# Optimization experiments

Measured on AMD Instinct MI355X. Metric: run time of the kernel, lower is better.

## Reference

```python
import jax, jax.numpy as jnp
import numpy as np
import math

B, NX, NY = 8, 1024, 1024
DIM_X = DIM_Y = DIM = 1024
H = 8


def layer_norm(x, g, b, eps=1e-5):
    mu = jnp.mean(x, axis=-1, keepdims=True)
    var = jnp.mean(jnp.square(x - mu), axis=-1, keepdims=True)
    return (x - mu) * jax.lax.rsqrt(var + eps) * g + b


def setup_inputs() -> dict:
    key = jax.random.key(0)
    ks = jax.random.split(key, 12)
    s = 1.0 / math.sqrt(DIM)
    return {
        "X": jax.random.normal(ks[0], (B, NX, DIM_X), jnp.float32),
        "Y": jax.random.normal(ks[1], (B, NY, DIM_Y), jnp.float32),
        "mask": jax.random.bernoulli(ks[2], 0.1, (B, NY)),  # True = masked out
        "Wq": jax.random.normal(ks[3], (DIM_X, DIM), jnp.float32) * s,
        "bq": jnp.zeros((DIM,), jnp.float32),
        "Wk": jax.random.normal(ks[4], (DIM_Y, DIM), jnp.float32) * s,
        "bk": jnp.zeros((DIM,), jnp.float32),
        "Wv": jax.random.normal(ks[5], (DIM_Y, DIM), jnp.float32) * s,
        "bv": jnp.zeros((DIM,), jnp.float32),
        "Wo": jax.random.normal(ks[6], (DIM, DIM), jnp.float32) * s,
        "bo": jnp.zeros((DIM,), jnp.float32),
        "g1": jnp.ones((DIM,), jnp.float32),
        "b1": jnp.zeros((DIM,), jnp.float32),
        "g2": jnp.ones((DIM,), jnp.float32),
        "b2": jnp.zeros((DIM,), jnp.float32),
    }


def reference(X, Y, mask, Wq, bq, Wk, bk, Wv, bv, Wo, bo, g1, b1, g2, b2):
    Q = X @ Wq + bq            # [B, NX, DIM]
    K = Y @ Wk + bk            # [B, NY, DIM]
    V = Y @ Wv + bv            # [B, NY, DIM]
    Dh = DIM // H
    Qh = Q.reshape(B, NX, H, Dh)
    Kh = K.reshape(B, NY, H, Dh)
    Vh = V.reshape(B, NY, H, Dh)
    # NOTE: original scales by sqrt(dim) (full model dim), not sqrt(head_dim)
    logits = jnp.einsum("bqhd,bkhd->bhqk", Qh, Kh) / math.sqrt(DIM)
    logits = jnp.where(mask[:, None, None, :], -jnp.inf, logits)
    A = jax.nn.softmax(logits, axis=-1)
    A = jnp.where(jnp.isnan(A), 0.0, A)  # fully-masked rows -> 0
    attn = jnp.einsum("bhqk,bkhd->bqhd", A, Vh).reshape(B, NX, DIM)
    O = layer_norm(Q + attn, g1, b1)
    O = layer_norm(O + jax.nn.relu(O @ Wo + bo), g2, b2)
    return O
```

## Files before the change

### kernel.cpp

```cpp
#include <hip/hip_runtime.h>
#include <stdint.h>


typedef unsigned short u16;
typedef unsigned int u32;
typedef __attribute__((ext_vector_type(8))) short s16x8;
typedef __attribute__((ext_vector_type(4))) float f32x4;
typedef __attribute__((ext_vector_type(16))) float f32x16;
typedef __attribute__((ext_vector_type(4))) u16 u16x4;

typedef __attribute__((address_space(1))) const void* as1cv;
typedef __attribute__((address_space(3))) void* as3v;

#define DEVINL __device__ __forceinline__

DEVINL u16 f2bf(float f) {
  union { float f; u32 u; } v; v.f = f;
  return (u16)((v.u + 0x7FFFu + ((v.u >> 16) & 1u)) >> 16);
}
DEVINL float bf2f(u16 x) {
  union { u32 u; float f; } v; v.u = ((u32)x) << 16;
  return v.f;
}
DEVINL u32 cvtpk_bf16(float lo, float hi) {
  u32 r;
  asm("v_cvt_pk_bf16_f32 %0, %1, %2" : "=v"(r) : "v"(lo), "v"(hi));
  return r;
}
DEVINL float fexp2(float x) {
  float r;
  asm("v_exp_f32 %0, %1" : "=v"(r) : "v"(x));
  return r;
}
DEVINL void gload_lds16(const void* g, void* l) {
  __builtin_amdgcn_global_load_lds((as1cv)g, (as3v)l, 16, 0, 0);
}
DEVINL f32x4 mfma16(s16x8 a, s16x8 b, f32x4 c) {
  return __builtin_amdgcn_mfma_f32_16x16x32_bf16(a, b, c, 0, 0, 0);
}
DEVINL f32x16 mfma32(s16x8 a, s16x8 b, f32x16 c) {
  return __builtin_amdgcn_mfma_f32_32x32x16_bf16(a, b, c, 0, 0, 0);
}
template <int N> DEVINL void wait_vm() {
  asm volatile("s_waitcnt vmcnt(%0)" :: "i"(N) : "memory");
  __builtin_amdgcn_sched_barrier(0);
}
DEVINL void wait_lgkm0() {
  asm volatile("s_waitcnt lgkmcnt(0)" ::: "memory");
  __builtin_amdgcn_sched_barrier(0);
}
DEVINL void barrier_raw() {
  __builtin_amdgcn_sched_barrier(0);
  __builtin_amdgcn_s_barrier();
  __builtin_amdgcn_sched_barrier(0);
}

__global__ __launch_bounds__(256) void prep_all(
    const float* __restrict__ X, u16* __restrict__ Xbf,
    const float* __restrict__ Y, u16* __restrict__ Ybf,
    const float* __restrict__ W0, const float* __restrict__ W1,
    const float* __restrict__ W2, const float* __restrict__ W3,
    u16* __restrict__ T0, u16* __restrict__ T1,
    u16* __restrict__ T2, u16* __restrict__ T3,
    const u32* __restrict__ mraw, float* __restrict__ maskb) {
  const int bid = blockIdx.x;
  const int t = threadIdx.x;
  if (bid < 16384) {
    int i = bid * 256 + t;
    const float* in = X;
    u16* out = Xbf;
    if (i >= 2097152) { i -= 2097152; in = Y; out = Ybf; }
    float4 v = *(const float4*)(in + (size_t)i * 4);
    u16x4 o; o[0] = f2bf(v.x); o[1] = f2bf(v.y); o[2] = f2bf(v.z); o[3] = f2bf(v.w);
    *(u16x4*)(out + (size_t)i * 4) = o;
    return;
  }
  if (bid < 20480) {
    const int r = bid - 16384;
    const int z = r >> 10, tile = r & 1023;
    const int bx = tile & 31, by = tile >> 5;
    const float* W = (z == 0) ? W0 : (z == 1) ? W1 : (z == 2) ? W2 : W3;
    u16* T = (z == 0) ? T0 : (z == 1) ? T1 : (z == 2) ? T2 : T3;
    __shared__ float tl[32][33];
    const int tx = t & 31, ty = t >> 5;
    const int N0 = bx << 5, K0 = by << 5;
#pragma unroll
    for (int i = 0; i < 4; ++i)
      tl[ty + i * 8][tx] = W[(size_t)(K0 + ty + i * 8) * 1024 + N0 + tx];
    __syncthreads();
#pragma unroll
    for (int i = 0; i < 4; ++i)
      T[(size_t)(N0 + ty + i * 8) * 1024 + K0 + tx] = f2bf(tl[tx][ty + i * 8]);
    return;
  }
  __shared__ int mode;
  int fB = 0, fF = 0;
  for (int i = t; i < 2048; i += 256) {
    u32 v = mraw[i];
    if (v == 0x3F800000u) fF = 1;
    else if (v > 1u) fB = 1;
  }
  if (t == 0) mode = 0;
  __syncthreads();
  if (fB) atomicOr(&mode, 1);
  if (fF) atomicOr(&mode, 2);
  __syncthreads();
  const int md = mode;
  const int idx = (bid - 20480) * 256 + t;
  int v;
  if (md & 1)       v = ((const unsigned char*)mraw)[idx] != 0;
  else if (md & 2)  v = ((const float*)mraw)[idx] != 0.0f;
  else              v = ((const int*)mraw)[idx] != 0;
  maskb[idx] = v ? -3e30f : -11.54156032f;
}

#define GEMM_KLOOP                                                            \
  for (int kt = 0; kt < 16; ++kt) {                                           \
    s16x8 af0[4], bf0[4], af1[4], bf1[4];                                     \
    _Pragma("unroll")                                                         \
    for (int mi = 0; mi < 4; ++mi) {                                          \
      int row = wm * 64 + mi * 16 + lrow;                                     \
      int off = row * 128 + ((lk * 16) ^ ((row & 7) << 4));                   \
      af0[mi] = *(const s16x8*)((const char*)lA + off);                       \
    }                                                                         \
    _Pragma("unroll")                                                         \
    for (int ni = 0; ni < 4; ++ni) {                                          \
      int row = wn * 64 + ni * 16 + lrow;                                     \
      int off = row * 128 + ((lk * 16) ^ ((row & 7) << 4));                   \
      bf0[ni] = *(const s16x8*)((const char*)lB + off);                       \
    }                                                                         \
    _Pragma("unroll")                                                         \
    for (int mi = 0; mi < 4; ++mi)                                            \
      _Pragma("unroll")                                                       \
      for (int ni = 0; ni < 4; ++ni)                                          \
        acc[mi][ni] = mfma16(af0[mi], bf0[ni], acc[mi][ni]);                  \
    _Pragma("unroll")                                                         \
    for (int mi = 0; mi < 4; ++mi) {                                          \
      int row = wm * 64 + mi * 16 + lrow;                                     \
      int off = row * 128 + ((lk * 16 + 64) ^ ((row & 7) << 4));              \
      af1[mi] = *(const s16x8*)((const char*)lA + off);                       \
    }                                                                         \
    _Pragma("unroll")                                                         \
    for (int ni = 0; ni < 4; ++ni) {                                          \
      int row = wn * 64 + ni * 16 + lrow;                                     \
      int off = row * 128 + ((lk * 16 + 64) ^ ((row & 7) << 4));              \
      bf1[ni] = *(const s16x8*)((const char*)lB + off);                       \
    }                                                                         \
    wait_lgkm0();                                                             \
    barrier_raw();                                                            \
    if (kt < 15) {                                                            \
      const int kb = (kt + 1) * 128;                                          \
      _Pragma("unroll")                                                       \
      for (int c = 0; c < 4; ++c) {                                           \
        int row = (w * 4 + c) * 8 + sr;                                       \
        gload_lds16(gA + (size_t)row * 2048 + kb + scol,                      \
                    (char*)lA + (w * 4 + c) * 1024);                          \
        gload_lds16(gB + (size_t)row * 2048 + kb + scol,                      \
                    (char*)lB + (w * 4 + c) * 1024);                          \
      }                                                                       \
    }                                                                         \
    _Pragma("unroll")                                                         \
    for (int mi = 0; mi < 4; ++mi)                                            \
      _Pragma("unroll")                                                       \
      for (int ni = 0; ni < 4; ++ni)                                          \
        acc[mi][ni] = mfma16(af1[mi], bf1[ni], acc[mi][ni]);                  \
    __syncthreads();                                                          \
  }

#define GEMM_PROLOGUE                                                         \
  _Pragma("unroll")                                                           \
  for (int c = 0; c < 4; ++c) {                                               \
    int row = (w * 4 + c) * 8 + sr;                                           \
    gload_lds16(gA + (size_t)row * 2048 + scol, (char*)lA + (w * 4 + c) * 1024); \
    gload_lds16(gB + (size_t)row * 2048 + scol, (char*)lB + (w * 4 + c) * 1024); \
  }                                                                           \
  __syncthreads();

__global__ __launch_bounds__(256, 2) void gemm_qkv(
    const u16* __restrict__ Xbf, const u16* __restrict__ Ybf,
    const u16* __restrict__ Wqt, const u16* __restrict__ Wkt,
    const u16* __restrict__ Wvt,
    const float* __restrict__ bq, const float* __restrict__ bk,
    const float* __restrict__ bv,
    u16* __restrict__ Qbf, u16* __restrict__ Kbf, u16* __restrict__ Vt) {
  __shared__ u16 lA[128 * 64];
  __shared__ u16 lB[128 * 64];

  const int id = blockIdx.x;
  const int g = id >> 9;
  const int sub = id & 511;
  const int swz = (sub & 7) * 64 + (sub >> 3);
  const int mb = swz >> 3;
  const int nb = swz & 7;

  const u16* A    = (g == 0) ? Xbf : Ybf;
  const u16* Bt   = (g == 0) ? Wqt : (g == 1) ? Wkt : Wvt;
  const float* bias = (g == 0) ? bq : (g == 1) ? bk : bv;

  const int tid = threadIdx.x;
  const int w = tid >> 6, l = tid & 63;
  const int wm = w >> 1, wn = w & 1;
  const int lrow = l & 15, lk = l >> 4;
  const int sr = l >> 3;
  const int scol = ((l & 7) << 4) ^ (sr << 4);
  const char* gA = (const char*)A + (size_t)(mb * 128) * 2048;
  const char* gB = (const char*)Bt + (size_t)(nb * 128) * 2048;

  f32x4 acc[4][4];
#pragma unroll
  for (int i = 0; i < 4; ++i)
#pragma unroll
    for (int j = 0; j < 4; ++j) acc[i][j] = f32x4{0.f, 0.f, 0.f, 0.f};

  GEMM_PROLOGUE
  GEMM_KLOOP

  const int growb = mb * 128 + wm * 64;
  const int gcolb = nb * 128 + wn * 64;
  float bs[4];
#pragma unroll
  for (int ni = 0; ni < 4; ++ni) bs[ni] = bias[gcolb + ni * 16 + lrow];

  if (g == 2) {
#pragma unroll
    for (int mi = 0; mi < 4; ++mi) {
      const int grow0 = growb + mi * 16 + lk * 4;
#pragma unroll
      for (int ni = 0; ni < 4; ++ni) {
        const int gcol = gcolb + ni * 16 + lrow;
        u16x4 pk;
#pragma unroll
        for (int r = 0; r < 4; ++r) pk[r] = f2bf(acc[mi][ni][r] + bs[ni]);
        size_t flat = ((size_t)((grow0 >> 10) << 10) + gcol) * 1024 + (grow0 & 1023);
        *(u16x4*)(Vt + flat) = pk;
      }
    }
  } else {
    u16* outBF = g ? Kbf : Qbf;
#pragma unroll
    for (int mi = 0; mi < 4; ++mi) {
      const int grow0 = growb + mi * 16 + lk * 4;
#pragma unroll
      for (int ni = 0; ni < 4; ++ni) {
        const int gcol = gcolb + ni * 16 + lrow;
#pragma unroll
        for (int r = 0; r < 4; ++r)
          outBF[(size_t)(grow0 + r) * 1024 + gcol] = f2bf(acc[mi][ni][r] + bs[ni]);
      }
    }
  }
}

__global__ __launch_bounds__(256, 2) void gemm_o(
    const u16* __restrict__ A, const u16* __restrict__ Bt,
    const float* __restrict__ bias, u16* __restrict__ outBF,
    const u16* __restrict__ residBF) {
  __shared__ u16 lA[128 * 64];
  __shared__ u16 lB[128 * 64];

  const int id = blockIdx.x;
  const int swz = (id & 7) * 64 + (id >> 3);
  const int mb = swz >> 3;
  const int nb = swz & 7;

  const int tid = threadIdx.x;
  const int w = tid >> 6, l = tid & 63;
  const int wm = w >> 1, wn = w & 1;
  const int lrow = l & 15, lk = l >> 4;
  const int sr = l >> 3;
  const int scol = ((l & 7) << 4) ^ (sr << 4);
  const char* gA = (const char*)A + (size_t)(mb * 128) * 2048;
  const char* gB = (const char*)Bt + (size_t)(nb * 128) * 2048;

  f32x4 acc[4][4];
#pragma unroll
  for (int i = 0; i < 4; ++i)
#pragma unroll
    for (int j = 0; j < 4; ++j) acc[i][j] = f32x4{0.f, 0.f, 0.f, 0.f};

  GEMM_PROLOGUE
  GEMM_KLOOP

  const int growb = mb * 128 + wm * 64;
  const int gcolb = nb * 128 + wn * 64;
  float bs[4];
#pragma unroll
  for (int ni = 0; ni < 4; ++ni) bs[ni] = bias[gcolb + ni * 16 + lrow];

#pragma unroll
  for (int mi = 0; mi < 4; ++mi) {
    const int grow0 = growb + mi * 16 + lk * 4;
#pragma unroll
    for (int ni = 0; ni < 4; ++ni) {
      const int gcol = gcolb + ni * 16 + lrow;
#pragma unroll
      for (int r = 0; r < 4; ++r) {
        float v = acc[mi][ni][r] + bs[ni];
        size_t idx = (size_t)(grow0 + r) * 1024 + gcol;
        outBF[idx] = f2bf(bf2f(residBF[idx]) + fmaxf(v, 0.f));
      }
    }
  }
}

__global__ __launch_bounds__(256, 2) void attn_fwd(
    const u16* __restrict__ Qbf, const u16* __restrict__ Kbf,
    const u16* __restrict__ Vt, const float* __restrict__ maskb,
    u16* __restrict__ attnO) {
  __shared__ u16 lK[2][64 * 128];
  __shared__ u16 lV[128 * 64];
  __shared__ float lM[1024];

  const int id = blockIdx.x;
  const int xcd = id & 7, seq = id >> 3;
  const int bh = xcd * 8 + (seq >> 3);
  const int qb = seq & 7;
  const int b = bh >> 3, h = bh & 7;
  const int tid = threadIdx.x;
  const int w = tid >> 6, l = tid & 63;
  const int q32 = l & 31, hi = l >> 5;

  const u16* Qrow = Qbf + ((size_t)(b * 1024 + qb * 128 + w * 32 + q32)) * 1024 + h * 128;
  s16x8 qf[8];
#pragma unroll
  for (int dc = 0; dc < 8; ++dc) qf[dc] = *(const s16x8*)(Qrow + dc * 16 + hi * 8);

  const int srK = l >> 4, slK = l & 15;
  int soK[4], soV[4];
#pragma unroll
  for (int c = 0; c < 4; ++c) {
    int rowK = (w * 4 + c) * 4 + srK;
    soK[c] = rowK * 2048 + ((slK << 4) ^ ((rowK & 15) << 4));
    int pairid = (w * 4 + c) * 4 + (l >> 4);
    int u = (l & 15) ^ (pairid & 15);
    int d = pairid * 2 + (u >> 3);
    soV[c] = d * 2048 + (u & 7) * 16;
  }
  const char* pgK = (const char*)(Kbf + ((size_t)(b * 1024)) * 1024 + h * 128);
  const char* pgV = (const char*)(Vt + ((size_t)(b * 1024 + h * 128)) * 1024);

  const int bK = q32 * 256;
  const int swzK = (q32 & 15) << 4;
  const int hib = hi * 16;
  int loV[4];
#pragma unroll
  for (int c = 0; c < 4; ++c)
    loV[c] = (q32 >> 1) * 256 +
             (((((q32 & 1) << 3) | (c * 2 + hi)) ^ ((q32 >> 1) & 15)) << 4);

  if (w == 0) {
#pragma unroll
    for (int c = 0; c < 4; ++c)
      gload_lds16(maskb + b * 1024 + c * 256 + l * 4, (char*)lM + c * 1024);
  }
#pragma unroll
  for (int c = 0; c < 4; ++c)
    gload_lds16(pgK + soK[c], (char*)lK[0] + w * 4096 + c * 1024);

  float l_ = 0.f;
  f32x16 oacc[4];
#pragma unroll
  for (int i = 0; i < 4; ++i)
#pragma unroll
    for (int r = 0; r < 16; ++r) oacc[i][r] = 0.f;

  const float SCL = 0.04508422f;
  const char* pM0 = (const char*)lM + hi * 16;

#define STAGE_K(TN, BUF)                                                      \
  {                                                                           \
    const char* pk_ = pgK + (size_t)(TN)*131072;                              \
    _Pragma("unroll")                                                         \
    for (int c = 0; c < 4; ++c)                                               \
      gload_lds16(pk_ + soK[c], (char*)lK[BUF] + w * 4096 + c * 1024);        \
  }
#define STAGE_V(TN)                                                           \
  {                                                                           \
    const char* pv_ = pgV + (size_t)(TN)*128;                                 \
    _Pragma("unroll")                                                         \
    for (int c = 0; c < 4; ++c)                                               \
      gload_lds16(pv_ + soV[c], (char*)lV + w * 4096 + c * 1024);             \
  }

#define ATT_TILE(T, CUR, FIRST, LAST)                                         \
  {                                                                           \
    STAGE_V(T);                                                               \
    if (FIRST) { wait_vm<4>(); barrier_raw(); }                               \
    f32x16 sc[2];                                                             \
    _Pragma("unroll")                                                         \
    for (int kb = 0; kb < 2; ++kb)                                            \
      _Pragma("unroll")                                                       \
      for (int r = 0; r < 16; ++r) sc[kb][r] = 0.f;                           \
    __builtin_amdgcn_s_setprio(1);                                            \
    _Pragma("unroll")                                                         \
    for (int dc = 0; dc < 8; ++dc) {                                          \
      int offk = bK + (((dc * 32) | hib) ^ swzK);                             \
      _Pragma("unroll")                                                       \
      for (int kb = 0; kb < 2; ++kb) {                                        \
        s16x8 kf = *(const s16x8*)((const char*)lK[CUR] + offk + kb * 8192);  \
        sc[kb] = mfma32(kf, qf[dc], sc[kb]);                                  \
      }                                                                       \
    }                                                                         \
    __builtin_amdgcn_s_setprio(0);                                            \
    const char* pMa = pM0 + (T)*256;                                          \
    float rs = 0.f;                                                           \
    _Pragma("unroll")                                                         \
    for (int kb = 0; kb < 2; ++kb) {                                          \
      f32x4 mv[4];                                                            \
      _Pragma("unroll")                                                       \
      for (int g = 0; g < 4; ++g)                                             \
        mv[g] = *(const f32x4*)(pMa + kb * 128 + g * 32);                     \
      _Pragma("unroll")                                                       \
      for (int r = 0; r < 16; ++r) {                                          \
        float pe = fexp2(fmaf(sc[kb][r], SCL, mv[r >> 2][r & 3]));            \
        sc[kb][r] = pe;                                                       \
        rs += pe;                                                             \
      }                                                                       \
    }                                                                         \
    rs += __shfl_xor(rs, 32);                                                 \
    l_ += rs;                                                                 \
    if (!(LAST)) STAGE_K((T) + 1, (CUR) ^ 1);                                 \
    if (LAST) wait_vm<0>(); else wait_vm<4>();                                \
    barrier_raw();                                                            \
    _Pragma("unroll")                                                         \
    for (int kc = 0; kc < 4; ++kc) {                                          \
      const int kb = kc >> 1;                                                 \
      const int ra2 = (kc & 1) * 8;                                           \
      u32 x0 = cvtpk_bf16(sc[kb][ra2 + 0], sc[kb][ra2 + 1]);                  \
      u32 x1 = cvtpk_bf16(sc[kb][ra2 + 2], sc[kb][ra2 + 3]);                  \
      u32 y0 = cvtpk_bf16(sc[kb][ra2 + 4], sc[kb][ra2 + 5]);                  \
      u32 y1 = cvtpk_bf16(sc[kb][ra2 + 6], sc[kb][ra2 + 7]);                  \
      asm("v_permlane32_swap_b32 %0, %1" : "+v"(x0), "+v"(y0));               \
      asm("v_permlane32_swap_b32 %0, %1" : "+v"(x1), "+v"(y1));               \
      union { u32 u[4]; s16x8 v; } pa;                                        \
      pa.u[0] = x0; pa.u[1] = x1; pa.u[2] = y0; pa.u[3] = y1;                 \
      __builtin_amdgcn_s_setprio(1);                                          \
      _Pragma("unroll")                                                       \
      for (int nb = 0; nb < 4; ++nb) {                                        \
        s16x8 vb = *(const s16x8*)((const char*)lV + loV[kc] + nb * 4096);    \
        oacc[nb] = mfma32(pa.v, vb, oacc[nb]);                                \
      }                                                                       \
      __builtin_amdgcn_s_setprio(0);                                          \
    }                                                                         \
    if (!(LAST)) { wait_vm<0>(); barrier_raw(); }                             \
  }

  ATT_TILE(0, 0, true, false);
  for (int it = 0; it < 7; ++it) {
    ATT_TILE(2 * it + 1, 1, false, false);
    ATT_TILE(2 * it + 2, 0, false, false);
  }
  ATT_TILE(15, 1, false, true);
#undef ATT_TILE
#undef STAGE_K
#undef STAGE_V

  float inv = (l_ > 1e-20f) ? (1.0f / l_) : 0.f;
  u16* obase = attnO + ((size_t)(b * 1024 + qb * 128 + w * 32)) * 1024 + h * 128;
#pragma unroll
  for (int r = 0; r < 16; ++r) {
    int qr = (r & 3) + 8 * (r >> 2) + 4 * hi;
    float iv = __shfl(inv, qr);
#pragma unroll
    for (int nb = 0; nb < 4; ++nb)
      obase[(size_t)qr * 1024 + nb * 32 + q32] = f2bf(oacc[nb][r] * iv);
  }
}

__global__ __launch_bounds__(256) void ln_fused(
    const float* __restrict__ aF, const u16* __restrict__ aBF,
    const u16* __restrict__ baddBF, const float* __restrict__ g,
    const float* __restrict__ bt, float* __restrict__ outF,
    u16* __restrict__ outBF) {
  const int row = blockIdx.x;
  const int c = threadIdx.x << 2;
  const size_t base = (size_t)row * 1024 + c;
  float4 h;
  if (aF) {
    h = *(const float4*)(aF + base);
  } else {
    u16x4 u = *(const u16x4*)(aBF + base);
    h.x = bf2f(u[0]); h.y = bf2f(u[1]); h.z = bf2f(u[2]); h.w = bf2f(u[3]);
  }
  if (baddBF) {
    u16x4 u = *(const u16x4*)(baddBF + base);
    h.x += bf2f(u[0]); h.y += bf2f(u[1]); h.z += bf2f(u[2]); h.w += bf2f(u[3]);
  }
  float s = (h.x + h.y) + (h.z + h.w);
  float q = (h.x * h.x + h.y * h.y) + (h.z * h.z + h.w * h.w);
#pragma unroll
  for (int msk = 1; msk < 64; msk <<= 1) {
    s += __shfl_xor(s, msk);
    q += __shfl_xor(q, msk);
  }
  __shared__ float sh[8];
  const int w = threadIdx.x >> 6;
  if ((threadIdx.x & 63) == 0) { sh[w] = s; sh[4 + w] = q; }
  __syncthreads();
  s = (sh[0] + sh[1]) + (sh[2] + sh[3]);
  q = (sh[4] + sh[5]) + (sh[6] + sh[7]);
  const float mu = s * (1.f / 1024.f);
  const float var = q * (1.f / 1024.f) - mu * mu;
  const float rstd = rsqrtf(var + 1e-5f);
  const float4 gv = *(const float4*)(g + c);
  const float4 bv = *(const float4*)(bt + c);
  float4 o;
  o.x = (h.x - mu) * rstd * gv.x + bv.x;
  o.y = (h.y - mu) * rstd * gv.y + bv.y;
  o.z = (h.z - mu) * rstd * gv.z + bv.z;
  o.w = (h.w - mu) * rstd * gv.w + bv.w;
  if (outF) *(float4*)(outF + base) = o;
  if (outBF) {
    u16x4 ub; ub[0] = f2bf(o.x); ub[1] = f2bf(o.y); ub[2] = f2bf(o.z); ub[3] = f2bf(o.w);
    *(u16x4*)(outBF + base) = ub;
  }
}

extern "C" void kernel_launch(void* const* d_in, const int* in_sizes, int n_in,
                              void* d_out, int out_size, void* d_ws, size_t ws_size,
                              hipStream_t stream) {
  const float* X  = (const float*)d_in[0];
  const float* Y  = (const float*)d_in[1];
  const void*  mask = d_in[2];
  const float* Wq = (const float*)d_in[3];
  const float* bq = (const float*)d_in[4];
  const float* Wk = (const float*)d_in[5];
  const float* bk = (const float*)d_in[6];
  const float* Wv = (const float*)d_in[7];
  const float* bv = (const float*)d_in[8];
  const float* Wo = (const float*)d_in[9];
  const float* bo = (const float*)d_in[10];
  const float* g1 = (const float*)d_in[11];
  const float* b1 = (const float*)d_in[12];
  const float* g2 = (const float*)d_in[13];
  const float* b2 = (const float*)d_in[14];
  float* out = (float*)d_out;

  char* ws = (char*)d_ws;
  const size_t MB = 1024ull * 1024ull;
  u16* Xbf    = (u16*)(ws + 0);
  u16* Ybf    = (u16*)(ws + 16 * MB);
  u16* Qbf    = (u16*)(ws + 32 * MB);
  u16* Kbf    = (u16*)(ws + 48 * MB);
  u16* Vt     = (u16*)(ws + 64 * MB);
  u16* attnbf = (u16*)(ws + 80 * MB);
  u16* Wqt = (u16*)(ws + 112 * MB);
  u16* Wkt = (u16*)(ws + 114 * MB);
  u16* Wvt = (u16*)(ws + 116 * MB);
  u16* Wot = (u16*)(ws + 118 * MB);
  float* maskb = (float*)(ws + 120 * MB);
  u16* Rbf = Kbf;
  u16* O1bf = Xbf;

  prep_all<<<dim3(20512), dim3(256), 0, stream>>>(
      X, Xbf, Y, Ybf, Wq, Wk, Wv, Wo, Wqt, Wkt, Wvt, Wot,
      (const u32*)mask, maskb);

  gemm_qkv<<<dim3(1536), dim3(256), 0, stream>>>(
      Xbf, Ybf, Wqt, Wkt, Wvt, bq, bk, bv, Qbf, Kbf, Vt);

  attn_fwd<<<dim3(512), dim3(256), 0, stream>>>(Qbf, Kbf, Vt, maskb, attnbf);

  ln_fused<<<dim3(8192), dim3(256), 0, stream>>>(nullptr, Qbf, attnbf, g1, b1, nullptr, O1bf);
  gemm_o<<<dim3(512), dim3(256), 0, stream>>>(O1bf, Wot, bo, Rbf, O1bf);
  ln_fused<<<dim3(8192), dim3(256), 0, stream>>>(nullptr, Rbf, nullptr, g2, b2, out, nullptr);
}
```

Before: 170.0 us.

## Fuse fp32-to-bf16 conversion of X and Y into QKV GEMM A-tile loads

Removes the separate conversion pass that turned X and Y into bf16 workspace copies. The QKV GEMM now reads fp32 A tiles straight from global memory into registers, one stage ahead, and converts them to bf16 with packed cvt instructions before writing the swizzled LDS layout. B tiles still use direct global-to-LDS loads. This saves writing and re-reading 32MB of bf16 intermediates, at the cost of more register pressure and twice the A-side global reads for each of the 8 N-blocks.

Result: faster. 166.3 us (-2.1%).

```diff
diff --git a/kernel.cpp b/kernel.cpp
--- a/kernel.cpp
+++ b/kernel.cpp
@@ -8,6 +8,7 @@
 typedef __attribute__((ext_vector_type(4))) float f32x4;
 typedef __attribute__((ext_vector_type(16))) float f32x16;
 typedef __attribute__((ext_vector_type(4))) u16 u16x4;
+typedef __attribute__((ext_vector_type(4))) u32 u32x4;
 
 typedef __attribute__((address_space(1))) const void* as1cv;
 typedef __attribute__((address_space(3))) void* as3v;
@@ -56,8 +57,6 @@
 }
 
 __global__ __launch_bounds__(256) void prep_all(
-    const float* __restrict__ X, u16* __restrict__ Xbf,
-    const float* __restrict__ Y, u16* __restrict__ Ybf,
     const float* __restrict__ W0, const float* __restrict__ W1,
     const float* __restrict__ W2, const float* __restrict__ W3,
     u16* __restrict__ T0, u16* __restrict__ T1,
@@ -65,19 +64,8 @@
     const u32* __restrict__ mraw, float* __restrict__ maskb) {
   const int bid = blockIdx.x;
   const int t = threadIdx.x;
-  if (bid < 16384) {
-    int i = bid * 256 + t;
-    const float* in = X;
-    u16* out = Xbf;
-    if (i >= 2097152) { i -= 2097152; in = Y; out = Ybf; }
-    float4 v = *(const float4*)(in + (size_t)i * 4);
-    u16x4 o; o[0] = f2bf(v.x); o[1] = f2bf(v.y); o[2] = f2bf(v.z); o[3] = f2bf(v.w);
-    *(u16x4*)(out + (size_t)i * 4) = o;
-    return;
-  }
-  if (bid < 20480) {
-    const int r = bid - 16384;
-    const int z = r >> 10, tile = r & 1023;
+  if (bid < 4096) {
+    const int z = bid >> 10, tile = bid & 1023;
     const int bx = tile & 31, by = tile >> 5;
     const float* W = (z == 0) ? W0 : (z == 1) ? W1 : (z == 2) ? W2 : W3;
     u16* T = (z == 0) ? T0 : (z == 1) ? T1 : (z == 2) ? T2 : T3;
@@ -106,7 +94,7 @@
   if (fF) atomicOr(&mode, 2);
   __syncthreads();
   const int md = mode;
-  const int idx = (bid - 20480) * 256 + t;
+  const int idx = (bid - 4096) * 256 + t;
   int v;
   if (md & 1)       v = ((const unsigned char*)mraw)[idx] != 0;
   else if (md & 2)  v = ((const float*)mraw)[idx] != 0.0f;
@@ -114,70 +102,8 @@
   maskb[idx] = v ? -3e30f : -11.54156032f;
 }
 
-#define GEMM_KLOOP                                                            \
-  for (int kt = 0; kt < 16; ++kt) {                                           \
-    s16x8 af0[4], bf0[4], af1[4], bf1[4];                                     \
-    _Pragma("unroll")                                                         \
-    for (int mi = 0; mi < 4; ++mi) {                                          \
-      int row = wm * 64 + mi * 16 + lrow;                                     \
-      int off = row * 128 + ((lk * 16) ^ ((row & 7) << 4));                   \
-      af0[mi] = *(const s16x8*)((const char*)lA + off);                       \
-    }                                                                         \
-    _Pragma("unroll")                                                         \
-    for (int ni = 0; ni < 4; ++ni) {                                          \
-      int row = wn * 64 + ni * 16 + lrow;                                     \
-      int off = row * 128 + ((lk * 16) ^ ((row & 7) << 4));                   \
-      bf0[ni] = *(const s16x8*)((const char*)lB + off);                       \
-    }                                                                         \
-    _Pragma("unroll")                                                         \
-    for (int mi = 0; mi < 4; ++mi)                                            \
-      _Pragma("unroll")                                                       \
-      for (int ni = 0; ni < 4; ++ni)                                          \
-        acc[mi][ni] = mfma16(af0[mi], bf0[ni], acc[mi][ni]);                  \
-    _Pragma("unroll")                                                         \
-    for (int mi = 0; mi < 4; ++mi) {                                          \
-      int row = wm * 64 + mi * 16 + lrow;                                     \
-      int off = row * 128 + ((lk * 16 + 64) ^ ((row & 7) << 4));              \
-      af1[mi] = *(const s16x8*)((const char*)lA + off);                       \
-    }                                                                         \
-    _Pragma("unroll")                                                         \
-    for (int ni = 0; ni < 4; ++ni) {                                          \
-      int row = wn * 64 + ni * 16 + lrow;                                     \
-      int off = row * 128 + ((lk * 16 + 64) ^ ((row & 7) << 4));              \
-      bf1[ni] = *(const s16x8*)((const char*)lB + off);                       \
-    }                                                                         \
-    wait_lgkm0();                                                             \
-    barrier_raw();                                                            \
-    if (kt < 15) {                                                            \
-      const int kb = (kt + 1) * 128;                                          \
-      _Pragma("unroll")                                                       \
-      for (int c = 0; c < 4; ++c) {                                           \
-        int row = (w * 4 + c) * 8 + sr;                                       \
-        gload_lds16(gA + (size_t)row * 2048 + kb + scol,                      \
-                    (char*)lA + (w * 4 + c) * 1024);                          \
-        gload_lds16(gB + (size_t)row * 2048 + kb + scol,                      \
-                    (char*)lB + (w * 4 + c) * 1024);                          \
-      }                                                                       \
-    }                                                                         \
-    _Pragma("unroll")                                                         \
-    for (int mi = 0; mi < 4; ++mi)                                            \
-      _Pragma("unroll")                                                       \
-      for (int ni = 0; ni < 4; ++ni)                                          \
-        acc[mi][ni] = mfma16(af1[mi], bf1[ni], acc[mi][ni]);                  \
-    __syncthreads();                                                          \
-  }
-
-#define GEMM_PROLOGUE                                                         \
-  _Pragma("unroll")                                                           \
-  for (int c = 0; c < 4; ++c) {                                               \
-    int row = (w * 4 + c) * 8 + sr;                                           \
-    gload_lds16(gA + (size_t)row * 2048 + scol, (char*)lA + (w * 4 + c) * 1024); \
-    gload_lds16(gB + (size_t)row * 2048 + scol, (char*)lB + (w * 4 + c) * 1024); \
-  }                                                                           \
-  __syncthreads();
-
 __global__ __launch_bounds__(256, 2) void gemm_qkv(
-    const u16* __restrict__ Xbf, const u16* __restrict__ Ybf,
+    const float* __restrict__ X, const float* __restrict__ Y,
     const u16* __restrict__ Wqt, const u16* __restrict__ Wkt,
     const u16* __restrict__ Wvt,
     const float* __restrict__ bq, const float* __restrict__ bk,
@@ -193,9 +119,157 @@
   const int mb = swz >> 3;
   const int nb = swz & 7;
 
-  const u16* A    = (g == 0) ? Xbf : Ybf;
+  const float* Af = (g == 0) ? X : Y;
   const u16* Bt   = (g == 0) ? Wqt : (g == 1) ? Wkt : Wvt;
   const float* bias = (g == 0) ? bq : (g == 1) ? bk : bv;
+
+  const int tid = threadIdx.x;
+  const int w = tid >> 6, l = tid & 63;
+  const int wm = w >> 1, wn = w & 1;
+  const int lrow = l & 15, lk = l >> 4;
+
+  const int asr = l >> 3;
+  const int acol = (l & 7) * 32;
+  const int acb = (l & 7) * 16;
+  const int bscol = ((l & 7) << 4) ^ (asr << 4);
+  const char* gAf = (const char*)Af + (size_t)(mb * 128) * 4096;
+  const char* gB  = (const char*)Bt + (size_t)(nb * 128) * 2048;
+
+  f32x4 acc[4][4];
+#pragma unroll
+  for (int i = 0; i < 4; ++i)
+#pragma unroll
+    for (int j = 0; j < 4; ++j) acc[i][j] = f32x4{0.f, 0.f, 0.f, 0.f};
+
+#define QKV_A_ISSUE(KT)                                                       \
+  _Pragma("unroll")                                                           \
+  for (int c = 0; c < 4; ++c) {                                               \
+    const char* p = gAf + (size_t)((w * 4 + c) * 8 + asr) * 4096 +            \
+                    (size_t)(KT) * 256 + acol;                                \
+    ar[c][0] = *(const f32x4*)p;                                              \
+    ar[c][1] = *(const f32x4*)(p + 16);                                       \
+  }
+#define QKV_A_WRITE                                                           \
+  _Pragma("unroll")                                                           \
+  for (int c = 0; c < 4; ++c) {                                               \
+    const int row = (w * 4 + c) * 8 + asr;                                    \
+    u32x4 pw;                                                                 \
+    pw[0] = cvtpk_bf16(ar[c][0][0], ar[c][0][1]);                             \
+    pw[1] = cvtpk_bf16(ar[c][0][2], ar[c][0][3]);                             \
+    pw[2] = cvtpk_bf16(ar[c][1][0], ar[c][1][1]);                             \
+    pw[3] = cvtpk_bf16(ar[c][1][2], ar[c][1][3]);                             \
+    *(u32x4*)((char*)lA + row * 128 + (acb ^ ((row & 7) << 4))) = pw;         \
+  }
+#define QKV_B_STAGE(KT)                                                       \
+  _Pragma("unroll")                                                           \
+  for (int c = 0; c < 4; ++c) {                                               \
+    const int row = (w * 4 + c) * 8 + asr;                                    \
+    gload_lds16(gB + (size_t)row * 2048 + (size_t)(KT) * 128 + bscol,         \
+                (char*)lB + (w * 4 + c) * 1024);                              \
+  }
+
+  f32x4 ar[4][2];
+  QKV_A_ISSUE(0)
+  QKV_B_STAGE(0)
+  QKV_A_WRITE
+  __syncthreads();
+
+  for (int kt = 0; kt < 16; ++kt) {
+    s16x8 af0[4], bf0[4], af1[4], bf1[4];
+#pragma unroll
+    for (int mi = 0; mi < 4; ++mi) {
+      int row = wm * 64 + mi * 16 + lrow;
+      int off = row * 128 + ((lk * 16) ^ ((row & 7) << 4));
+      af0[mi] = *(const s16x8*)((const char*)lA + off);
+    }
+#pragma unroll
+    for (int ni = 0; ni < 4; ++ni) {
+      int row = wn * 64 + ni * 16 + lrow;
+      int off = row * 128 + ((lk * 16) ^ ((row & 7) << 4));
+      bf0[ni] = *(const s16x8*)((const char*)lB + off);
+    }
+    if (kt < 15) { QKV_A_ISSUE(kt + 1) }
+#pragma unroll
+    for (int mi = 0; mi < 4; ++mi)
+#pragma unroll
+      for (int ni = 0; ni < 4; ++ni)
+        acc[mi][ni] = mfma16(af0[mi], bf0[ni], acc[mi][ni]);
+#pragma unroll
+    for (int mi = 0; mi < 4; ++mi) {
+      int row = wm * 64 + mi * 16 + lrow;
+      int off = row * 128 + ((lk * 16 + 64) ^ ((row & 7) << 4));
+      af1[mi] = *(const s16x8*)((const char*)lA + off);
+    }
+#pragma unroll
+    for (int ni = 0; ni < 4; ++ni) {
+      int row = wn * 64 + ni * 16 + lrow;
+      int off = row * 128 + ((lk * 16 + 64) ^ ((row & 7) << 4));
+      bf1[ni] = *(const s16x8*)((const char*)lB + off);
+    }
+    wait_lgkm0();
+    barrier_raw();
+    if (kt < 15) {
+      QKV_B_STAGE(kt + 1)
+      QKV_A_WRITE
+    }
+#pragma unroll
+    for (int mi = 0; mi < 4; ++mi)
+#pragma unroll
+      for (int ni = 0; ni < 4; ++ni)
+        acc[mi][ni] = mfma16(af1[mi], bf1[ni], acc[mi][ni]);
+    __syncthreads();
+  }
+#undef QKV_A_ISSUE
+#undef QKV_A_WRITE
+#undef QKV_B_STAGE
+
+  const int growb = mb * 128 + wm * 64;
+  const int gcolb = nb * 128 + wn * 64;
+  float bs[4];
+#pragma unroll
+  for (int ni = 0; ni < 4; ++ni) bs[ni] = bias[gcolb + ni * 16 + lrow];
+
+  if (g == 2) {
+#pragma unroll
+    for (int mi = 0; mi < 4; ++mi) {
+      const int grow0 = growb + mi * 16 + lk * 4;
+#pragma unroll
+      for (int ni = 0; ni < 4; ++ni) {
+        const int gcol = gcolb + ni * 16 + lrow;
+        u16x4 pk;
+#pragma unroll
+        for (int r = 0; r < 4; ++r) pk[r] = f2bf(acc[mi][ni][r] + bs[ni]);
+        size_t flat = ((size_t)((grow0 >> 10) << 10) + gcol) * 1024 + (grow0 & 1023);
+        *(u16x4*)(Vt + flat) = pk;
+      }
+    }
+  } else {
+    u16* outBF = g ? Kbf : Qbf;
+#pragma unroll
+    for (int mi = 0; mi < 4; ++mi) {
+      const int grow0 = growb + mi * 16 + lk * 4;
+#pragma unroll
+      for (int ni = 0; ni < 4; ++ni) {
+        const int gcol = gcolb + ni * 16 + lrow;
+#pragma unroll
+        for (int r = 0; r < 4; ++r)
+          outBF[(size_t)(grow0 + r) * 1024 + gcol] = f2bf(acc[mi][ni][r] + bs[ni]);
+      }
+    }
+  }
+}
+
+__global__ __launch_bounds__(256, 2) void gemm_o(
+    const u16* __restrict__ A, const u16* __restrict__ Bt,
+    const float* __restrict__ bias, u16* __restrict__ outBF,
+    const u16* __restrict__ residBF) {
+  __shared__ u16 lA[128 * 64];
+  __shared__ u16 lB[128 * 64];
+
+  const int id = blockIdx.x;
+  const int swz = (id & 7) * 64 + (id >> 3);
+  const int mb = swz >> 3;
+  const int nb = swz & 7;
 
   const int tid = threadIdx.x;
   const int w = tid >> 6, l = tid & 63;
@@ -212,74 +286,63 @@
 #pragma unroll
     for (int j = 0; j < 4; ++j) acc[i][j] = f32x4{0.f, 0.f, 0.f, 0.f};
 
-  GEMM_PROLOGUE
-  GEMM_KLOOP
-
-  const int growb = mb * 128 + wm * 64;
-  const int gcolb = nb * 128 + wn * 64;
-  float bs[4];
-#pragma unroll
-  for (int ni = 0; ni < 4; ++ni) bs[ni] = bias[gcolb + ni * 16 + lrow];
-
-  if (g == 2) {
+#pragma unroll
+  for (int c = 0; c < 4; ++c) {
+    int row = (w * 4 + c) * 8 + sr;
+    gload_lds16(gA + (size_t)row * 2048 + scol, (char*)lA + (w * 4 + c) * 1024);
+    gload_lds16(gB + (size_t)row * 2048 + scol, (char*)lB + (w * 4 + c) * 1024);
+  }
+  __syncthreads();
+
+  for (int kt = 0; kt < 16; ++kt) {
+    s16x8 af0[4], bf0[4], af1[4], bf1[4];
 #pragma unroll
     for (int mi = 0; mi < 4; ++mi) {
-      const int grow0 = growb + mi * 16 + lk * 4;
-#pragma unroll
-      for (int ni = 0; ni < 4; ++ni) {
-        const int gcol = gcolb + ni * 16 + lrow;
-        u16x4 pk;
-#pragma unroll
-        for (int r = 0; r < 4; ++r) pk[r] = f2bf(acc[mi][ni][r] + bs[ni]);
-        size_t flat = ((size_t)((grow0 >> 10) << 10) + gcol) * 1024 + (grow0 & 1023);
-        *(u16x4*)(Vt + flat) = pk;
+      int row = wm * 64 + mi * 16 + lrow;
+      int off = row * 128 + ((lk * 16) ^ ((row & 7) << 4));
+      af0[mi] = *(const s16x8*)((const char*)lA + off);
+    }
+#pragma unroll
+    for (int ni = 0; ni < 4; ++ni) {
+      int row = wn * 64 + ni * 16 + lrow;
+      int off = row * 128 + ((lk * 16) ^ ((row & 7) << 4));
+      bf0[ni] = *(const s16x8*)((const char*)lB + off);
+    }
+#pragma unroll
+    for (int mi = 0; mi < 4; ++mi)
+#pragma unroll
+      for (int ni = 0; ni < 4; ++ni)
+        acc[mi][ni] = mfma16(af0[mi], bf0[ni], acc[mi][ni]);
+#pragma unroll
+    for (int mi = 0; mi < 4; ++mi) {
+      int row = wm * 64 + mi * 16 + lrow;
+      int off = row * 128 + ((lk * 16 + 64) ^ ((row & 7) << 4));
+      af1[mi] = *(const s16x8*)((const char*)lA + off);
+    }
+#pragma unroll
+    for (int ni = 0; ni < 4; ++ni) {
+      int row = wn * 64 + ni * 16 + lrow;
+      int off = row * 128 + ((lk * 16 + 64) ^ ((row & 7) << 4));
+      bf1[ni] = *(const s16x8*)((const char*)lB + off);
+    }
+    wait_lgkm0();
+    barrier_raw();
+    if (kt < 15) {
+      const int kb = (kt + 1) * 128;
+#pragma unroll
+      for (int c = 0; c < 4; ++c) {
+        int row = (w * 4 + c) * 8 + sr;
+        gload_lds16(gA + (size_t)row * 2048 + kb + scol, (char*)lA + (w * 4 + c) * 1024);
+        gload_lds16(gB + (size_t)row * 2048 + kb + scol, (char*)lB + (w * 4 + c) * 1024);
       }
     }
-  } else {
-    u16* outBF = g ? Kbf : Qbf;
-#pragma unroll
-    for (int mi = 0; mi < 4; ++mi) {
-      const int grow0 = growb + mi * 16 + lk * 4;
-#pragma unroll
-      for (int ni = 0; ni < 4; ++ni) {
-        const int gcol = gcolb + ni * 16 + lrow;
-#pragma unroll
-        for (int r = 0; r < 4; ++r)
-          outBF[(size_t)(grow0 + r) * 1024 + gcol] = f2bf(acc[mi][ni][r] + bs[ni]);
-      }
-    }
-  }
-}
-
-__global__ __launch_bounds__(256, 2) void gemm_o(
-    const u16* __restrict__ A, const u16* __restrict__ Bt,
-    const float* __restrict__ bias, u16* __restrict__ outBF,
-    const u16* __restrict__ residBF) {
-  __shared__ u16 lA[128 * 64];
-  __shared__ u16 lB[128 * 64];
-
-  const int id = blockIdx.x;
-  const int swz = (id & 7) * 64 + (id >> 3);
-  const int mb = swz >> 3;
-  const int nb = swz & 7;
-
-  const int tid = threadIdx.x;
-  const int w = tid >> 6, l = tid & 63;
-  const int wm = w >> 1, wn = w & 1;
-  const int lrow = l & 15, lk = l >> 4;
-  const int sr = l >> 3;
-  const int scol = ((l & 7) << 4) ^ (sr << 4);
-  const char* gA = (const char*)A + (size_t)(mb * 128) * 2048;
-  const char* gB = (const char*)Bt + (size_t)(nb * 128) * 2048;
-
-  f32x4 acc[4][4];
-#pragma unroll
-  for (int i = 0; i < 4; ++i)
-#pragma unroll
-    for (int j = 0; j < 4; ++j) acc[i][j] = f32x4{0.f, 0.f, 0.f, 0.f};
-
-  GEMM_PROLOGUE
-  GEMM_KLOOP
+#pragma unroll
+    for (int mi = 0; mi < 4; ++mi)
+#pragma unroll
+      for (int ni = 0; ni < 4; ++ni)
+        acc[mi][ni] = mfma16(af1[mi], bf1[ni], acc[mi][ni]);
+    __syncthreads();
+  }
 
   const int growb = mb * 128 + wm * 64;
   const int gcolb = nb * 128 + wn * 64;
@@ -538,8 +601,7 @@
 
   char* ws = (char*)d_ws;
   const size_t MB = 1024ull * 1024ull;
-  u16* Xbf    = (u16*)(ws + 0);
-  u16* Ybf    = (u16*)(ws + 16 * MB);
+  u16* O1bf   = (u16*)(ws + 0);
   u16* Qbf    = (u16*)(ws + 32 * MB);
   u16* Kbf    = (u16*)(ws + 48 * MB);
   u16* Vt     = (u16*)(ws + 64 * MB);
@@ -550,14 +612,12 @@
   u16* Wot = (u16*)(ws + 118 * MB);
   float* maskb = (float*)(ws + 120 * MB);
   u16* Rbf = Kbf;
-  u16* O1bf = Xbf;
-
-  prep_all<<<dim3(20512), dim3(256), 0, stream>>>(
-      X, Xbf, Y, Ybf, Wq, Wk, Wv, Wo, Wqt, Wkt, Wvt, Wot,
-      (const u32*)mask, maskb);
+
+  prep_all<<<dim3(4128), dim3(256), 0, stream>>>(
+      Wq, Wk, Wv, Wo, Wqt, Wkt, Wvt, Wot, (const u32*)mask, maskb);
 
   gemm_qkv<<<dim3(1536), dim3(256), 0, stream>>>(
-      Xbf, Ybf, Wqt, Wkt, Wvt, bq, bk, bv, Qbf, Kbf, Vt);
+      X, Y, Wqt, Wkt, Wvt, bq, bk, bv, Qbf, Kbf, Vt);
 
   attn_fwd<<<dim3(512), dim3(256), 0, stream>>>(Qbf, Kbf, Vt, maskb, attnbf);
 
```
